# Optimization experiments

Measured on AMD Instinct MI355X. Metric: run time of the kernel, lower is better.

## Reference

```python
import jax, jax.numpy as jnp
import numpy as np

EMBED = 512
HEADS = 8                      # num_heads
HD = EMBED // HEADS // 2       # diff-attn head dim = 32
EXP = 4
DEPTH = 1
LAMBDA_INIT = 0.8 - 0.6 * float(np.exp(-0.3 * (DEPTH - 1)))  # 0.2
EPS = 1e-5


def layernorm(x, w, b):
    mu = jnp.mean(x, axis=-1, keepdims=True)
    var = jnp.mean(jnp.square(x - mu), axis=-1, keepdims=True)
    return (x - mu) * jax.lax.rsqrt(var + EPS) * w + b


def rmsnorm(x, w):
    ms = jnp.mean(jnp.square(x), axis=-1, keepdims=True)
    return x * jax.lax.rsqrt(ms + EPS) * w


def setup_inputs() -> dict:
    key = jax.random.key(0)
    ks = jax.random.split(key, 12)
    B, N, D = 8, 1024, EMBED
    s = 0.02
    inp = {
        "x": jax.random.normal(ks[0], (B, N, D), jnp.float32),
        # diff-attention params
        "Wq": jax.random.normal(ks[1], (D, D), jnp.float32) * s,
        "Wk": jax.random.normal(ks[2], (D, D), jnp.float32) * s,
        "Wv": jax.random.normal(ks[3], (D, D), jnp.float32) * s,
        "Wo": jax.random.normal(ks[4], (D, D), jnp.float32) * s,
        "lq1": jax.random.normal(ks[5], (HD,), jnp.float32) * 0.1,
        "lk1": jax.random.normal(ks[6], (HD,), jnp.float32) * 0.1,
        "lq2": jax.random.normal(ks[7], (HD,), jnp.float32) * 0.1,
        "lk2": jax.random.normal(ks[8], (HD,), jnp.float32) * 0.1,
        "subln_w": jnp.ones((2 * HD,), jnp.float32),
        # block norms
        "n1_w": jnp.ones((D,), jnp.float32), "n1_b": jnp.zeros((D,), jnp.float32),
        "n2_w": jnp.ones((D,), jnp.float32), "n2_b": jnp.zeros((D,), jnp.float32),
        # MLP: LN(D) -> Linear(D,4D) -> GELU -> LN(4D) -> Linear(4D,D)
        "mln1_w": jnp.ones((D,), jnp.float32), "mln1_b": jnp.zeros((D,), jnp.float32),
        "mW1": jax.random.normal(ks[9], (EXP * D, D), jnp.float32) * s,
        "mb1": jnp.zeros((EXP * D,), jnp.float32),
        "mln2_w": jnp.ones((EXP * D,), jnp.float32), "mln2_b": jnp.zeros((EXP * D,), jnp.float32),
        "mW2": jax.random.normal(ks[10], (D, EXP * D), jnp.float32) * s,
        "mb2": jnp.zeros((D,), jnp.float32),
    }
    return inp


def diff_attn(x, Wq, Wk, Wv, Wo, lq1, lk1, lq2, lk2, subln_w):
    B, N, D = x.shape
    q = (x @ Wq.T).reshape(B, N, 2 * HEADS, HD).transpose(0, 2, 1, 3)   # [B,2H,N,hd]
    k = (x @ Wk.T).reshape(B, N, 2 * HEADS, HD).transpose(0, 2, 1, 3)   # [B,2H,N,hd]
    v = (x @ Wv.T).reshape(B, N, HEADS, 2 * HD).transpose(0, 2, 1, 3)   # [B,H,N,2hd]
    q = q * (HD ** -0.5)
    scores = jnp.einsum("bhnd,bhmd->bhnm", q, k)                        # [B,2H,N,N]
    attn = jax.nn.softmax(scores, axis=-1)
    attn = attn.reshape(B, HEADS, 2, N, N)
    lam1 = jnp.exp(jnp.sum(lq1 * lk1))
    lam2 = jnp.exp(jnp.sum(lq2 * lk2))
    lam = lam1 - lam2 + LAMBDA_INIT
    attn = attn[:, :, 0] - lam * attn[:, :, 1]                          # [B,H,N,N]
    out = jnp.einsum("bhnm,bhmd->bhnd", attn, v)                        # [B,H,N,2hd]
    out = rmsnorm(out, subln_w) * (1.0 - LAMBDA_INIT)
    out = out.transpose(0, 2, 1, 3).reshape(B, N, D)
    return out @ Wo.T


def reference(x, Wq, Wk, Wv, Wo, lq1, lk1, lq2, lk2, subln_w,
              n1_w, n1_b, n2_w, n2_b,
              mln1_w, mln1_b, mW1, mb1, mln2_w, mln2_b, mW2, mb2):
    x_res = x
    xn = layernorm(x, n1_w, n1_b)
    a = diff_attn(xn, Wq, Wk, Wv, Wo, lq1, lk1, lq2, lk2, subln_w)
    h = layernorm(a, n2_w, n2_b) + x_res
    # MLP
    z = layernorm(h, mln1_w, mln1_b)
    z = jax.nn.gelu(z @ mW1.T + mb1, approximate=False)
    z = layernorm(z, mln2_w, mln2_b)
    z = z @ mW2.T + mb2
    return z + h
```

## Files before the change

### kernel.cpp

```cpp
#include <hip/hip_runtime.h>
#include <cstdint>
#include <cstddef>

typedef unsigned short u16;
typedef unsigned int   u32;
typedef __attribute__((ext_vector_type(8))) short short8;
typedef __attribute__((ext_vector_type(4))) float floatx4;

__device__ __forceinline__ float asf(u32 u){ union{u32 u; float f;} v; v.u=u; return v.f; }
__device__ __forceinline__ u32 asu(float f){ union{float f; u32 u;} v; v.f=f; return v.u; }
__device__ __forceinline__ float bf2f(u16 u){ return asf(((u32)u)<<16); }
__device__ __forceinline__ u16 f2bf(float f){ u32 u = asu(f); u32 r = u + 0x7FFFu + ((u>>16)&1u); return (u16)(r>>16); }
__device__ __forceinline__ u16 f2bf_fast(float f){ return (u16)((asu(f) + 0x8000u)>>16); }
__device__ __forceinline__ u32 pack2(float a, float b){ return (u32)f2bf(a) | (((u32)f2bf(b))<<16); }
__device__ __forceinline__ void bf8f(uint4 d, float* o){
  o[0]=asf(d.x<<16); o[1]=asf(d.x&0xFFFF0000u);
  o[2]=asf(d.y<<16); o[3]=asf(d.y&0xFFFF0000u);
  o[4]=asf(d.z<<16); o[5]=asf(d.z&0xFFFF0000u);
  o[6]=asf(d.w<<16); o[7]=asf(d.w&0xFFFF0000u);
}
__device__ __forceinline__ float gelu_fast(float x){
  const float t = fminf(2.30220771f*(x + 0.044715f*x*x*x), 126.f);
  const float e = __builtin_amdgcn_exp2f(t);
  return x * e / (e + 1.f);
}

#define SC2 0.25503485966f

__global__ __launch_bounds__(256) void cvt_all(
    const float* __restrict__ Wq, const float* __restrict__ Wk,
    const float* __restrict__ Wv, const float* __restrict__ Wo,
    const float* __restrict__ W1, const float* __restrict__ W2,
    u16* __restrict__ Wqkv, u16* __restrict__ Wob,
    u16* __restrict__ W1b, u16* __restrict__ W2b)
{
  const int blk = blockIdx.x;
  const float* src; u16* dst; int off;
  if      (blk < 128)  { src = Wq; dst = Wqkv;          off = blk; }
  else if (blk < 256)  { src = Wk; dst = Wqkv + 262144; off = blk - 128; }
  else if (blk < 384)  { src = Wv; dst = Wqkv + 524288; off = blk - 256; }
  else if (blk < 512)  { src = Wo; dst = Wob;           off = blk - 384; }
  else if (blk < 1024) { src = W1; dst = W1b;           off = blk - 512; }
  else                 { src = W2; dst = W2b;           off = blk - 1024; }
  const int i = (off*256 + threadIdx.x)*8;
  const float4 a = *(const float4*)(src + i);
  const float4 b = *(const float4*)(src + i + 4);
  uint4 st;
  st.x = pack2(a.x, a.y); st.y = pack2(a.z, a.w);
  st.z = pack2(b.x, b.y); st.w = pack2(b.z, b.w);
  *(uint4*)(dst + i) = st;
}

enum { EPI_NONE=0, EPI_BIAS_GELU=1, EPI_BIAS_RES=2, EPI_QSCALE=3 };

template<int BM, int EPI, typename OutT>
__global__ __launch_bounds__(256) void gemm_bt(
    const u16* __restrict__ A, const u16* __restrict__ B,
    const float* __restrict__ bias, const void* __restrict__ res,
    OutT* __restrict__ C, int M, int N, int K)
{
  static_assert(BM == 64, "vmcnt literal assumes 3 loads/stage (BM=64)");
  __shared__ u16 As[3][BM*32];
  __shared__ u16 Bs[3][128*32];
  const int tid  = threadIdx.x;
  const int wave = tid >> 6;
  const int lane = tid & 63;
  const int bm = blockIdx.y, bn = blockIdx.x;

  const int srow = wave*16 + (lane>>2);
  const int scol = (lane&3)*8;
  const u16* Ag = A + (size_t)bm*BM*K;
  const u16* Bg = B + (size_t)bn*128*K;

  constexpr int WM = BM/2;
  constexpr int MI = WM/16;
  const int wm = (wave>>1)*WM;
  const int wn = (wave&1)*64;
  const int fr = lane & 15;
  const int fk = (lane>>4)*8;

  floatx4 acc[MI][4] = {};

  #define G_STAGE(buf, kk)                                                        \
    do {                                                                          \
      __builtin_amdgcn_global_load_lds(                                           \
          (__attribute__((address_space(1))) void*)(Ag + (size_t)srow*K + (kk) + scol), \
          (__attribute__((address_space(3))) void*)(&As[buf][wave*16*32]),        \
          16, 0, 0);                                                              \
      _Pragma("unroll")                                                           \
      for (int tt = 0; tt < 2; ++tt)                                              \
        __builtin_amdgcn_global_load_lds(                                         \
            (__attribute__((address_space(1))) void*)(Bg + (size_t)(tt*64 + srow)*K + (kk) + scol), \
            (__attribute__((address_space(3))) void*)(&Bs[buf][(tt*64 + wave*16)*32]),      \
            16, 0, 0);                                                            \
    } while (0)

  G_STAGE(0, 0);

  const int nsteps = K >> 5;
  for (int s = 0; s < nsteps; ++s) {
    const int cur = s % 3;
    if (s + 1 < nsteps) {
      G_STAGE((s+1)%3, (s+1)*32);
      asm volatile("s_waitcnt vmcnt(3)" ::: "memory");
    } else {
      asm volatile("s_waitcnt vmcnt(0)" ::: "memory");
    }
    __builtin_amdgcn_s_barrier();
    __builtin_amdgcn_sched_barrier(0);

    short8 af[MI], bfr[4];
    #pragma unroll
    for (int i=0;i<MI;i++) af[i] = *(const short8*)(&As[cur][(wm + i*16 + fr)*32 + fk]);
    #pragma unroll
    for (int j=0;j<4;j++) bfr[j] = *(const short8*)(&Bs[cur][(wn + j*16 + fr)*32 + fk]);
    #pragma unroll
    for (int i=0;i<MI;i++)
      #pragma unroll
      for (int j=0;j<4;j++)
        acc[i][j] = __builtin_amdgcn_mfma_f32_16x16x32_bf16(af[i], bfr[j], acc[i][j], 0, 0, 0);
  }
  #undef G_STAGE

  const int col0 = bn*128 + wn + fr;
  float bv[4] = {0.f,0.f,0.f,0.f};
  if constexpr (EPI == EPI_BIAS_GELU || EPI == EPI_BIAS_RES) {
    #pragma unroll
    for (int j=0;j<4;j++) bv[j] = bias[col0 + j*16];
  }
  const u16* r16 = (const u16*)res;
  const int rq = (lane>>4)*4;
  #pragma unroll
  for (int i=0;i<MI;i++){
    #pragma unroll
    for (int rr=0;rr<4;rr++){
      const int m = bm*BM + wm + i*16 + rq + rr;
      const size_t rowoff = (size_t)m*N;
      #pragma unroll
      for (int j=0;j<4;j++){
        float vv = acc[i][j][rr];
        const int n = col0 + j*16;
        if constexpr (EPI == EPI_BIAS_GELU){
          vv = gelu_fast(vv + bv[j]);
        } else if constexpr (EPI == EPI_BIAS_RES){
          vv += bv[j] + bf2f(r16[rowoff + n]);
        } else if constexpr (EPI == EPI_QSCALE){
          if (n < 512) vv *= SC2;
        }
        if constexpr (sizeof(OutT) == 2) C[rowoff + n] = f2bf(vv);
        else                             C[rowoff + n] = vv;
      }
    }
  }
}

__global__ __launch_bounds__(256) void ln512_kernel(
    const float* __restrict__ x, const float* __restrict__ w, const float* __restrict__ b,
    u16* __restrict__ out)
{
  const int row  = blockIdx.x*4 + (threadIdx.x>>6);
  const int lane = threadIdx.x & 63;
  const size_t base = (size_t)row*512 + lane*8;
  float v[8];
  { const float4 a = *(const float4*)(x + base);
    const float4 c = *(const float4*)(x + base + 4);
    v[0]=a.x; v[1]=a.y; v[2]=a.z; v[3]=a.w; v[4]=c.x; v[5]=c.y; v[6]=c.z; v[7]=c.w; }
  float s=0.f, sq=0.f;
  #pragma unroll
  for (int i=0;i<8;i++){ s += v[i]; sq += v[i]*v[i]; }
  for (int off=32; off>0; off>>=1){ s += __shfl_xor(s, off, 64); sq += __shfl_xor(sq, off, 64); }
  const float mu = s*(1.f/512.f);
  const float rs = rsqrtf(sq*(1.f/512.f) - mu*mu + 1e-5f);
  float o[8];
  #pragma unroll
  for (int i=0;i<8;i++)
    o[i] = (v[i]-mu)*rs*w[lane*8+i] + b[lane*8+i];
  uint4 st; st.x=pack2(o[0],o[1]); st.y=pack2(o[2],o[3]); st.z=pack2(o[4],o[5]); st.w=pack2(o[6],o[7]);
  *(uint4*)(out + base) = st;
}

__global__ __launch_bounds__(256) void lnres_kernel(
    const u16* __restrict__ ao, const float* __restrict__ x,
    const float* __restrict__ w2, const float* __restrict__ b2,
    const float* __restrict__ w3, const float* __restrict__ b3,
    u16* __restrict__ h, u16* __restrict__ z)
{
  const int row  = blockIdx.x*4 + (threadIdx.x>>6);
  const int lane = threadIdx.x & 63;
  const size_t base = (size_t)row*512 + lane*8;
  float a[8], xr[8];
  bf8f(*(const uint4*)(ao + base), a);
  { const float4 p = *(const float4*)(x + base);
    const float4 q = *(const float4*)(x + base + 4);
    xr[0]=p.x; xr[1]=p.y; xr[2]=p.z; xr[3]=p.w; xr[4]=q.x; xr[5]=q.y; xr[6]=q.z; xr[7]=q.w; }
  float s=0.f, sq=0.f;
  #pragma unroll
  for (int i=0;i<8;i++){ s += a[i]; sq += a[i]*a[i]; }
  for (int off=32; off>0; off>>=1){ s += __shfl_xor(s, off, 64); sq += __shfl_xor(sq, off, 64); }
  float mu = s*(1.f/512.f);
  float rs = rsqrtf(sq*(1.f/512.f) - mu*mu + 1e-5f);
  float hv[8];
  #pragma unroll
  for (int i=0;i<8;i++)
    hv[i] = (a[i]-mu)*rs*w2[lane*8+i] + b2[lane*8+i] + xr[i];
  { uint4 st; st.x=pack2(hv[0],hv[1]); st.y=pack2(hv[2],hv[3]);
    st.z=pack2(hv[4],hv[5]); st.w=pack2(hv[6],hv[7]);
    *(uint4*)(h + base) = st; }
  s=0.f; sq=0.f;
  #pragma unroll
  for (int i=0;i<8;i++){ s += hv[i]; sq += hv[i]*hv[i]; }
  for (int off=32; off>0; off>>=1){ s += __shfl_xor(s, off, 64); sq += __shfl_xor(sq, off, 64); }
  mu = s*(1.f/512.f);
  rs = rsqrtf(sq*(1.f/512.f) - mu*mu + 1e-5f);
  float zv[8];
  #pragma unroll
  for (int i=0;i<8;i++)
    zv[i] = (hv[i]-mu)*rs*w3[lane*8+i] + b3[lane*8+i];
  uint4 st; st.x=pack2(zv[0],zv[1]); st.y=pack2(zv[2],zv[3]); st.z=pack2(zv[4],zv[5]); st.w=pack2(zv[6],zv[7]);
  *(uint4*)(z + base) = st;
}

__global__ __launch_bounds__(256) void ln2048_kernel(
    const u16* x, const float* __restrict__ w, const float* __restrict__ b,
    u16* out)
{
  const int row  = blockIdx.x*4 + (threadIdx.x>>6);
  const int lane = threadIdx.x & 63;
  const u16* xp = x + (size_t)row*2048;
  float v[32];
  #pragma unroll
  for (int g=0; g<4; ++g) bf8f(*(const uint4*)(xp + g*512 + lane*8), v + g*8);
  float s=0.f, sq=0.f;
  #pragma unroll
  for (int i=0;i<32;i++){ s += v[i]; sq += v[i]*v[i]; }
  for (int off=32; off>0; off>>=1){ s += __shfl_xor(s, off, 64); sq += __shfl_xor(sq, off, 64); }
  const float mu = s*(1.f/2048.f);
  const float rs = rsqrtf(sq*(1.f/2048.f) - mu*mu + 1e-5f);
  u16* op = out + (size_t)row*2048;
  #pragma unroll
  for (int g=0; g<4; ++g){
    float o[8];
    #pragma unroll
    for (int i=0;i<8;i++){
      const int idx = g*512 + lane*8 + i;
      o[i] = (v[g*8+i]-mu)*rs*w[idx] + b[idx];
    }
    uint4 st; st.x=pack2(o[0],o[1]); st.y=pack2(o[2],o[3]); st.z=pack2(o[4],o[5]); st.w=pack2(o[6],o[7]);
    *(uint4*)(op + g*512 + lane*8) = st;
  }
}

__global__ __launch_bounds__(256) void transpose_v(
    const u16* __restrict__ QKV, u16* __restrict__ Vt)
{
  __shared__ __align__(16) u16 T[64][72];
  const int bid = blockIdx.x;
  const int bh  = bid >> 4;
  const int kt  = bid & 15;
  const int b   = bh >> 3;
  const int h   = bh & 7;
  const int tid = threadIdx.x;

  const int key = tid >> 2;
  const int dc  = (tid & 3) * 16;
  const u16* src = QKV + ((size_t)(b*1024 + kt*64 + key))*1536 + 1024 + h*64 + dc;
  const uint4 a0 = *(const uint4*)(src);
  const uint4 a1 = *(const uint4*)(src + 8);
  *(uint4*)(&T[key][dc])     = a0;
  *(uint4*)(&T[key][dc + 8]) = a1;
  __syncthreads();

  const int d  = tid >> 2;
  const int kc = (tid & 3) * 16;
  union { uint4 q[2]; u16 us[16]; } ow;
  #pragma unroll
  for (int i=0;i<16;i++) ow.us[i] = T[kc + i][d];
  u16* dst = Vt + ((size_t)(bh*64 + d))*1024 + kt*64 + kc;
  *(uint4*)(dst)     = ow.q[0];
  *(uint4*)(dst + 8) = ow.q[1];
}

__global__ __launch_bounds__(256) void attn_mfma(
    const u16* __restrict__ QKV, const u16* __restrict__ Vt,
    const float* __restrict__ lq1, const float* __restrict__ lk1,
    const float* __restrict__ lq2, const float* __restrict__ lk2,
    const float* __restrict__ subw, u16* __restrict__ out)
{
  __shared__ __align__(16) u16 Ks1[2][64*32];
  __shared__ __align__(16) u16 Ks2[2][64*32];
  __shared__ __align__(16) u16 Vs [2][64*64];
  __shared__ __align__(16) u16 Ps [4][16*32];

  const int tid  = threadIdx.x;
  const int wave = tid >> 6;
  const int lane = tid & 63;
  const int quad = lane >> 4;
  const int l15  = lane & 15;

  const int bid = blockIdx.x;
  const int bh  = (bid & 7)*8 + ((bid >> 3) >> 4);
  const int qt  = (bid >> 3) & 15;
  const int b   = bh >> 3;
  const int h   = bh & 7;

  float t1 = 0.f, t2 = 0.f;
  for (int i=0;i<32;i++){ t1 += lq1[i]*lk1[i]; t2 += lq2[i]*lk2[i]; }
  const float lam = __expf(t1) - __expf(t2) + 0.2f;

  const int qrowg = b*1024 + qt*64 + wave*16 + l15;
  const short8 aq1 = *(const short8*)(QKV + (size_t)qrowg*1536 + 2*h*32 + quad*8);
  const short8 aq2 = *(const short8*)(QKV + (size_t)qrowg*1536 + 2*h*32 + 32 + quad*8);

  floatx4 O1[4] = {}, O2[4] = {};
  float l1acc[4] = {0.f,0.f,0.f,0.f};
  float l2acc[4] = {0.f,0.f,0.f,0.f};
  const floatx4 zf4 = {0.f,0.f,0.f,0.f};

  const int kvbase = b*1024;
  u16* pw = &Ps[wave][0];

  const int kchunk = ((lane&3) ^ ((lane>>3)&3)) * 8;
  const u16* KbaseS = QKV + (size_t)(kvbase + wave*16 + (lane>>2))*1536 + 512 + 2*h*32 + kchunk;
  const int vchunk = ((lane&7) ^ (lane>>3)) * 8;
  const u16* VbaseS = Vt + ((size_t)bh*64 + wave*16 + (lane>>3))*1024 + vchunk;

  #define STAGE_TILE(buf, tt)                                                     \
    do {                                                                          \
      const u16* kp = KbaseS + (size_t)(tt)*64*1536;                              \
      __builtin_amdgcn_global_load_lds(                                           \
          (__attribute__((address_space(1))) void*)(kp),                          \
          (__attribute__((address_space(3))) void*)(&Ks1[buf][wave*16*32]), 16, 0, 0); \
      __builtin_amdgcn_global_load_lds(                                           \
          (__attribute__((address_space(1))) void*)(kp + 32),                     \
          (__attribute__((address_space(3))) void*)(&Ks2[buf][wave*16*32]), 16, 0, 0); \
      const u16* vp = VbaseS + (tt)*64;                                           \
      __builtin_amdgcn_global_load_lds(                                           \
          (__attribute__((address_space(1))) void*)(vp),                          \
          (__attribute__((address_space(3))) void*)(&Vs[buf][wave*16*64]), 16, 0, 0); \
      __builtin_amdgcn_global_load_lds(                                           \
          (__attribute__((address_space(1))) void*)(vp + (size_t)8*1024),         \
          (__attribute__((address_space(3))) void*)(&Vs[buf][(wave*16+8)*64]), 16, 0, 0); \
    } while (0)

  STAGE_TILE(0, 0);
  __syncthreads();

  const int kslotR = (quad ^ ((l15>>1)&3)) * 8;
  const int pslotR = ((quad + (l15>>2)) & 3) * 8;

  for (int t = 0; t < 16; ++t) {
    const int cur = t & 1;

    if (t < 15) STAGE_TILE(cur^1, t+1);

    #pragma unroll
    for (int kh = 0; kh < 2; ++kh) {
      u32 p2h[4];
      #pragma unroll
      for (int ktl = 0; ktl < 2; ++ktl) {
        const int kt = kh*2 + ktl;
        const short8 bk1 = *(const short8*)(&Ks1[cur][(kt*16 + l15)*32 + kslotR]);
        const short8 bk2 = *(const short8*)(&Ks2[cur][(kt*16 + l15)*32 + kslotR]);
        const floatx4 s1 = __builtin_amdgcn_mfma_f32_16x16x32_bf16(aq1, bk1, zf4, 0, 0, 0);
        const floatx4 s2 = __builtin_amdgcn_mfma_f32_16x16x32_bf16(aq2, bk2, zf4, 0, 0, 0);
        const int wslot = ((ktl*2 + (l15>>3) + quad) & 3)*8;
        u16* d1 = pw + wslot + (l15&7);
        float p2v[4];
        #pragma unroll
        for (int rr = 0; rr < 4; ++rr) {
          const float p1 = __builtin_amdgcn_exp2f(s1[rr]);
          const float p2 = __builtin_amdgcn_exp2f(s2[rr]);
          d1[(quad*4+rr)*32] = f2bf_fast(p1);
          l1acc[rr] += p1;
          l2acc[rr] += p2;
          p2v[rr] = p2;
        }
        p2h[ktl*2+0] = (u32)f2bf_fast(p2v[0]) | ((u32)f2bf_fast(p2v[1])<<16);
        p2h[ktl*2+1] = (u32)f2bf_fast(p2v[2]) | ((u32)f2bf_fast(p2v[3])<<16);
      }
      const short8 ap1 = *(const short8*)(pw + l15*32 + pslotR);
      #pragma unroll
      for (int ktl = 0; ktl < 2; ++ktl) {
        const int wslot = ((ktl*2 + (l15>>3) + quad) & 3)*8;
        u16* d2 = pw + wslot + (l15&7);
        d2[(quad*4+0)*32] = (u16)(p2h[ktl*2+0] & 0xFFFFu);
        d2[(quad*4+1)*32] = (u16)(p2h[ktl*2+0] >> 16);
        d2[(quad*4+2)*32] = (u16)(p2h[ktl*2+1] & 0xFFFFu);
        d2[(quad*4+3)*32] = (u16)(p2h[ktl*2+1] >> 16);
      }
      const short8 ap2 = *(const short8*)(pw + l15*32 + pslotR);
      const int vslotR = ((kh*4 + quad) ^ (l15&7)) * 8;
      #pragma unroll
      for (int nt = 0; nt < 4; ++nt) {
        const short8 bv = *(const short8*)(&Vs[cur][(nt*16 + l15)*64 + vslotR]);
        O1[nt] = __builtin_amdgcn_mfma_f32_16x16x32_bf16(ap1, bv, O1[nt], 0, 0, 0);
        O2[nt] = __builtin_amdgcn_mfma_f32_16x16x32_bf16(ap2, bv, O2[nt], 0, 0, 0);
      }
    }

    if (t < 15) __syncthreads();
  }
  #undef STAGE_TILE

  #pragma unroll
  for (int rr=0; rr<4; ++rr){
    float v1 = l1acc[rr], v2 = l2acc[rr];
    v1 += __shfl_xor(v1, 1, 64); v2 += __shfl_xor(v2, 1, 64);
    v1 += __shfl_xor(v1, 2, 64); v2 += __shfl_xor(v2, 2, 64);
    v1 += __shfl_xor(v1, 4, 64); v2 += __shfl_xor(v2, 4, 64);
    v1 += __shfl_xor(v1, 8, 64); v2 += __shfl_xor(v2, 8, 64);
    l1acc[rr] = v1; l2acc[rr] = v2;
  }

  float sw[4];
  #pragma unroll
  for (int nt=0; nt<4; ++nt) sw[nt] = subw[nt*16 + l15];

  #pragma unroll
  for (int rr=0; rr<4; ++rr){
    const int row = quad*4 + rr;
    const float il1 = 1.f / l1acc[rr];
    const float cl2 = lam / l2acc[rr];
    float o[4]; float ss = 0.f;
    #pragma unroll
    for (int nt=0; nt<4; ++nt){
      o[nt] = O1[nt][rr]*il1 - O2[nt][rr]*cl2;
      ss += o[nt]*o[nt];
    }
    ss += __shfl_xor(ss, 1, 64);
    ss += __shfl_xor(ss, 2, 64);
    ss += __shfl_xor(ss, 4, 64);
    ss += __shfl_xor(ss, 8, 64);
    const float rs = rsqrtf(ss*(1.f/64.f) + 1e-5f) * 0.8f;
    const int orow = b*1024 + qt*64 + wave*16 + row;
    u16* op = out + (size_t)orow*512 + h*64 + l15;
    #pragma unroll
    for (int nt=0; nt<4; ++nt)
      op[nt*16] = f2bf_fast(o[nt]*rs*sw[nt]);
  }
}

extern "C" void kernel_launch(void* const* d_in, const int* in_sizes, int n_in,
                              void* d_out, int out_size, void* d_ws, size_t ws_size,
                              hipStream_t stream)
{
  (void)in_sizes; (void)n_in; (void)out_size; (void)ws_size;
  const float* x    = (const float*)d_in[0];
  const float* Wq   = (const float*)d_in[1];
  const float* Wk   = (const float*)d_in[2];
  const float* Wv   = (const float*)d_in[3];
  const float* Wo   = (const float*)d_in[4];
  const float* lq1  = (const float*)d_in[5];
  const float* lk1  = (const float*)d_in[6];
  const float* lq2  = (const float*)d_in[7];
  const float* lk2  = (const float*)d_in[8];
  const float* subw = (const float*)d_in[9];
  const float* n1w  = (const float*)d_in[10];
  const float* n1b  = (const float*)d_in[11];
  const float* n2w  = (const float*)d_in[12];
  const float* n2b  = (const float*)d_in[13];
  const float* m1w  = (const float*)d_in[14];
  const float* m1b  = (const float*)d_in[15];
  const float* mW1  = (const float*)d_in[16];
  const float* mb1  = (const float*)d_in[17];
  const float* m2w  = (const float*)d_in[18];
  const float* m2b  = (const float*)d_in[19];
  const float* mW2  = (const float*)d_in[20];
  const float* mb2  = (const float*)d_in[21];
  float* out = (float*)d_out;

  char* ws = (char*)d_ws;
  const size_t MB = (size_t)1 << 20;
  u16*  xn  = (u16*)(ws + 0*MB);
  u16*  qkv = (u16*)(ws + 8*MB);
  u16*  a   = (u16*)(ws + 0*MB);
  u16*  ao  = (u16*)(ws + 8*MB);
  u16*  z1  = (u16*)(ws + 16*MB);
  u16*  vt  = (u16*)(ws + 32*MB);
  u16*  hb  = (u16*)(ws + 40*MB);
  u16*  t   = (u16*)(ws + 48*MB);
  u16* Wqkvb= (u16*)(ws + 80*MB);
  u16* Wob  = (u16*)(ws + 81*MB + 512*1024);
  u16* W1b  = (u16*)(ws + 82*MB);
  u16* W2b  = (u16*)(ws + 84*MB);

  const int M = 8192;

  cvt_all<<<1536, 256, 0, stream>>>(Wq, Wk, Wv, Wo, mW1, mW2, Wqkvb, Wob, W1b, W2b);

  ln512_kernel<<<2048, 256, 0, stream>>>(x, n1w, n1b, xn);

  gemm_bt<64,EPI_QSCALE,u16><<<dim3(12,128), 256, 0, stream>>>(xn, Wqkvb, nullptr, nullptr, qkv, M, 1536, 512);

  transpose_v<<<1024, 256, 0, stream>>>(qkv, vt);

  attn_mfma<<<1024, 256, 0, stream>>>(qkv, vt, lq1, lk1, lq2, lk2, subw, a);

  gemm_bt<64,EPI_NONE,u16><<<dim3(4,128), 256, 0, stream>>>(a, Wob, nullptr, nullptr, ao, M, 512, 512);

  lnres_kernel<<<2048, 256, 0, stream>>>(ao, x, n2w, n2b, m1w, m1b, hb, z1);

  gemm_bt<64,EPI_BIAS_GELU,u16><<<dim3(16,128), 256, 0, stream>>>(z1, W1b, mb1, nullptr, t, M, 2048, 512);

  ln2048_kernel<<<2048, 256, 0, stream>>>(t, m2w, m2b, t);

  gemm_bt<64,EPI_BIAS_RES,float><<<dim3(4,128), 256, 0, stream>>>(t, W2b, mb2, hb, out, M, 512, 2048);
}
```

Measured before the change: 311.5 us.

## Fold 2048-wide LayerNorm into the final GEMM via precomputed weight sums

Instead of normalizing the 2048-wide MLP hidden tensor and writing it back, the change computes only per-row mean and rstd, pre-scales W2 by the LN weight, and precomputes per-column sums of W2·w and W2·b plus bias. The final GEMM epilogue applies rs*(acc - mu*c1) + c2 + residual. This drops a full read-modify-write of the 32 MB bf16 intermediate and adds a small reduction kernel plus extra epilogue loads. It also changes numerics, since the GEMM now runs on un-normalized bf16 GELU outputs and the mean is subtracted after accumulation, which risks cancellation error.

```diff
diff --git a/kernel.cpp b/kernel.cpp
--- a/kernel.cpp
+++ b/kernel.cpp
@@ -31,32 +31,67 @@
     const float* __restrict__ Wq, const float* __restrict__ Wk,
     const float* __restrict__ Wv, const float* __restrict__ Wo,
     const float* __restrict__ W1, const float* __restrict__ W2,
+    const float* __restrict__ w3,
     u16* __restrict__ Wqkv, u16* __restrict__ Wob,
     u16* __restrict__ W1b, u16* __restrict__ W2b)
 {
   const int blk = blockIdx.x;
-  const float* src; u16* dst; int off;
+  const float* src; u16* dst; int off; bool scale = false;
   if      (blk < 128)  { src = Wq; dst = Wqkv;          off = blk; }
   else if (blk < 256)  { src = Wk; dst = Wqkv + 262144; off = blk - 128; }
   else if (blk < 384)  { src = Wv; dst = Wqkv + 524288; off = blk - 256; }
   else if (blk < 512)  { src = Wo; dst = Wob;           off = blk - 384; }
   else if (blk < 1024) { src = W1; dst = W1b;           off = blk - 512; }
-  else                 { src = W2; dst = W2b;           off = blk - 1024; }
+  else                 { src = W2; dst = W2b;           off = blk - 1024; scale = true; }
   const int i = (off*256 + threadIdx.x)*8;
-  const float4 a = *(const float4*)(src + i);
-  const float4 b = *(const float4*)(src + i + 4);
+  float4 a = *(const float4*)(src + i);
+  float4 b = *(const float4*)(src + i + 4);
+  if (scale) {
+    const int k = i & 2047;
+    const float4 wa = *(const float4*)(w3 + k);
+    const float4 wb = *(const float4*)(w3 + k + 4);
+    a.x*=wa.x; a.y*=wa.y; a.z*=wa.z; a.w*=wa.w;
+    b.x*=wb.x; b.y*=wb.y; b.z*=wb.z; b.w*=wb.w;
+  }
   uint4 st;
   st.x = pack2(a.x, a.y); st.y = pack2(a.z, a.w);
   st.z = pack2(b.x, b.y); st.w = pack2(b.z, b.w);
   *(uint4*)(dst + i) = st;
 }
 
-enum { EPI_NONE=0, EPI_BIAS_GELU=1, EPI_BIAS_RES=2, EPI_QSCALE=3 };
+__global__ __launch_bounds__(256) void c12_kernel(
+    const float* __restrict__ W2, const float* __restrict__ w3,
+    const float* __restrict__ b3, const float* __restrict__ mb2,
+    float* __restrict__ cbuf)
+{
+  const int n    = blockIdx.x*4 + (threadIdx.x>>6);
+  const int lane = threadIdx.x & 63;
+  const float* row = W2 + (size_t)n*2048 + lane*32;
+  const float* w3p = w3 + lane*32;
+  const float* b3p = b3 + lane*32;
+  float s1 = 0.f, s2 = 0.f;
+  #pragma unroll
+  for (int i = 0; i < 32; i += 4) {
+    const float4 wv = *(const float4*)(row + i);
+    const float4 av = *(const float4*)(w3p + i);
+    const float4 bv = *(const float4*)(b3p + i);
+    s1 += wv.x*av.x + wv.y*av.y + wv.z*av.z + wv.w*av.w;
+    s2 += wv.x*bv.x + wv.y*bv.y + wv.z*bv.z + wv.w*bv.w;
+  }
+  for (int off = 32; off > 0; off >>= 1) {
+    s1 += __shfl_xor(s1, off, 64);
+    s2 += __shfl_xor(s2, off, 64);
+  }
+  if (lane == 0) { cbuf[2*n] = s1; cbuf[2*n+1] = s2 + mb2[n]; }
+}
+
+enum { EPI_NONE=0, EPI_BIAS_GELU=1, EPI_BIAS_RES=2, EPI_QSCALE=3, EPI_LNFOLD=4 };
 
 template<int BM, int EPI, typename OutT>
 __global__ __launch_bounds__(256) void gemm_bt(
     const u16* __restrict__ A, const u16* __restrict__ B,
     const float* __restrict__ bias, const void* __restrict__ res,
+    const float* __restrict__ stats,
     OutT* __restrict__ C, int M, int N, int K)
 {
   static_assert(BM == 64, "vmcnt literal assumes 3 loads/stage (BM=64)");
@@ -124,9 +159,13 @@
 
   const int col0 = bn*128 + wn + fr;
   float bv[4] = {0.f,0.f,0.f,0.f};
+  float c2v[4] = {0.f,0.f,0.f,0.f};
   if constexpr (EPI == EPI_BIAS_GELU || EPI == EPI_BIAS_RES) {
     #pragma unroll
     for (int j=0;j<4;j++) bv[j] = bias[col0 + j*16];
+  } else if constexpr (EPI == EPI_LNFOLD) {
+    #pragma unroll
+    for (int j=0;j<4;j++){ bv[j] = bias[2*(col0 + j*16)]; c2v[j] = bias[2*(col0 + j*16)+1]; }
   }
   const u16* r16 = (const u16*)res;
   const int rq = (lane>>4)*4;
@@ -136,6 +175,8 @@
     for (int rr=0;rr<4;rr++){
       const int m = bm*BM + wm + i*16 + rq + rr;
       const size_t rowoff = (size_t)m*N;
+      float mu = 0.f, rs = 0.f;
+      if constexpr (EPI == EPI_LNFOLD){ mu = stats[2*m]; rs = stats[2*m+1]; }
       #pragma unroll
       for (int j=0;j<4;j++){
         float vv = acc[i][j][rr];
@@ -146,6 +187,8 @@
           vv += bv[j] + bf2f(r16[rowoff + n]);
         } else if constexpr (EPI == EPI_QSCALE){
           if (n < 512) vv *= SC2;
+        } else if constexpr (EPI == EPI_LNFOLD){
+          vv = rs*(vv - mu*bv[j]) + c2v[j] + bf2f(r16[rowoff + n]);
         }
         if constexpr (sizeof(OutT) == 2) C[rowoff + n] = f2bf(vv);
         else                             C[rowoff + n] = vv;
@@ -220,9 +263,8 @@
   *(uint4*)(z + base) = st;
 }
 
-__global__ __launch_bounds__(256) void ln2048_kernel(
-    const u16* x, const float* __restrict__ w, const float* __restrict__ b,
-    u16* out)
+__global__ __launch_bounds__(256) void ln2048_stats(
+    const u16* __restrict__ x, float* __restrict__ sbuf)
 {
   const int row  = blockIdx.x*4 + (threadIdx.x>>6);
   const int lane = threadIdx.x & 63;
@@ -236,18 +278,7 @@
   for (int off=32; off>0; off>>=1){ s += __shfl_xor(s, off, 64); sq += __shfl_xor(sq, off, 64); }
   const float mu = s*(1.f/2048.f);
   const float rs = rsqrtf(sq*(1.f/2048.f) - mu*mu + 1e-5f);
-  u16* op = out + (size_t)row*2048;
-  #pragma unroll
-  for (int g=0; g<4; ++g){
-    float o[8];
-    #pragma unroll
-    for (int i=0;i<8;i++){
-      const int idx = g*512 + lane*8 + i;
-      o[i] = (v[g*8+i]-mu)*rs*w[idx] + b[idx];
-    }
-    uint4 st; st.x=pack2(o[0],o[1]); st.y=pack2(o[2],o[3]); st.z=pack2(o[4],o[5]); st.w=pack2(o[6],o[7]);
-    *(uint4*)(op + g*512 + lane*8) = st;
-  }
+  if (lane == 0) { sbuf[2*row] = mu; sbuf[2*row+1] = rs; }
 }
 
 __global__ __launch_bounds__(256) void transpose_v(
@@ -483,26 +514,30 @@
   u16* Wob  = (u16*)(ws + 81*MB + 512*1024);
   u16* W1b  = (u16*)(ws + 82*MB);
   u16* W2b  = (u16*)(ws + 84*MB);
+  float* sbuf = (float*)(ws + 86*MB);
+  float* cbuf = (float*)(ws + 86*MB + 65536);
 
   const int M = 8192;
 
-  cvt_all<<<1536, 256, 0, stream>>>(Wq, Wk, Wv, Wo, mW1, mW2, Wqkvb, Wob, W1b, W2b);
+  cvt_all<<<1536, 256, 0, stream>>>(Wq, Wk, Wv, Wo, mW1, mW2, m2w, Wqkvb, Wob, W1b, W2b);
+
+  c12_kernel<<<128, 256, 0, stream>>>(mW2, m2w, m2b, mb2, cbuf);
 
   ln512_kernel<<<2048, 256, 0, stream>>>(x, n1w, n1b, xn);
 
-  gemm_bt<64,EPI_QSCALE,u16><<<dim3(12,128), 256, 0, stream>>>(xn, Wqkvb, nullptr, nullptr, qkv, M, 1536, 512);
+  gemm_bt<64,EPI_QSCALE,u16><<<dim3(12,128), 256, 0, stream>>>(xn, Wqkvb, nullptr, nullptr, nullptr, qkv, M, 1536, 512);
 
   transpose_v<<<1024, 256, 0, stream>>>(qkv, vt);
 
   attn_mfma<<<1024, 256, 0, stream>>>(qkv, vt, lq1, lk1, lq2, lk2, subw, a);
 
-  gemm_bt<64,EPI_NONE,u16><<<dim3(4,128), 256, 0, stream>>>(a, Wob, nullptr, nullptr, ao, M, 512, 512);
+  gemm_bt<64,EPI_NONE,u16><<<dim3(4,128), 256, 0, stream>>>(a, Wob, nullptr, nullptr, nullptr, ao, M, 512, 512);
 
   lnres_kernel<<<2048, 256, 0, stream>>>(ao, x, n2w, n2b, m1w, m1b, hb, z1);
 
-  gemm_bt<64,EPI_BIAS_GELU,u16><<<dim3(16,128), 256, 0, stream>>>(z1, W1b, mb1, nullptr, t, M, 2048, 512);
-
-  ln2048_kernel<<<2048, 256, 0, stream>>>(t, m2w, m2b, t);
-
-  gemm_bt<64,EPI_BIAS_RES,float><<<dim3(4,128), 256, 0, stream>>>(t, W2b, mb2, hb, out, M, 512, 2048);
-}
+  gemm_bt<64,EPI_BIAS_GELU,u16><<<dim3(16,128), 256, 0, stream>>>(z1, W1b, mb1, nullptr, nullptr, t, M, 2048, 512);
+
+  ln2048_stats<<<2048, 256, 0, stream>>>(t, sbuf);
+
+  gemm_bt<64,EPI_LNFOLD,float><<<dim3(4,128), 256, 0, stream>>>(t, W2b, cbuf, hb, sbuf, out, M, 512, 2048);
+}
```

Result: no change. 307.0 us (-1.4%).
